# Performance work log

Hardware: AMD Instinct MI355X
Metric: run time of the kernel (lower is better)

## Reference

```python
import jax, jax.numpy as jnp
import numpy as np

MARGIN = 0.1
LAMDA = 1.0


def setup_inputs() -> dict:
    key = jax.random.key(0)
    k1, k2, k3 = jax.random.split(key, 3)
    B, C, D = 256, 4096, 100
    return {
        "feat_pos": jax.random.normal(k1, (B, D), dtype=jnp.float32),
        "feat_neg": jax.random.normal(k2, (B, C, D), dtype=jnp.float32),
        "feat_lan": jax.random.normal(k3, (B, D), dtype=jnp.float32),
    }


def reference(feat_pos, feat_neg, feat_lan):
    # loss1: overall mean squared distance between pos and lang features
    loss1 = jnp.mean((feat_pos - feat_lan) ** 2)
    # loss2: hinge on per-(b,c) mean squared distance pos vs each neg clip
    # d2[b, c] = mean_d (pos[b, d] - neg[b, c, d])^2
    d2 = jnp.mean((feat_pos[:, None, :] - feat_neg) ** 2, axis=-1)  # (B, C)
    loss2 = jnp.mean(jax.nn.relu(MARGIN - d2))  # sum / (B*C)
    return loss1 + LAMDA * loss2
```

## Files before the change

### kernel.cpp

```cpp
#include <hip/hip_runtime.h>

#define MARGIN 0.1f
#define BB 256
#define CC 4096
#define DD 100
#define TPB 256

__global__ __launch_bounds__(TPB) void amloss_kernel(const float* __restrict__ pos,
                                                     const float* __restrict__ neg,
                                                     const float* __restrict__ lan,
                                                     float* __restrict__ out) {
    const int tid = threadIdx.x;
    const int b   = blockIdx.y;
    const int c   = blockIdx.x * TPB + tid;

    __shared__ __align__(16) float pos_s[DD];
    if (tid < DD) pos_s[tid] = pos[b * DD + tid];
    __syncthreads();

    const float4* __restrict__ row =
        (const float4*)(neg + ((size_t)b * CC + (size_t)c) * DD);
    const float4* __restrict__ pos4 = (const float4*)pos_s;

    float s = 0.f;
    #pragma unroll
    for (int k = 0; k < DD / 4; ++k) {
        const float4 v = row[k];
        const float4 p = pos4[k];
        const float d0 = p.x - v.x;
        const float d1 = p.y - v.y;
        const float d2 = p.z - v.z;
        const float d3 = p.w - v.w;
        s += d0 * d0 + d1 * d1 + d2 * d2 + d3 * d3;
    }
    float contrib = fmaxf(MARGIN - s * (1.f / (float)DD), 0.f)
                  * (1.f / ((float)BB * (float)CC));

    if (blockIdx.x == 0 && tid < DD) {
        const float d = pos_s[tid] - lan[b * DD + tid];
        contrib += d * d * (1.f / ((float)BB * (float)DD));
    }

    #pragma unroll
    for (int off = 32; off >= 1; off >>= 1)
        contrib += __shfl_xor(contrib, off, 64);
    __shared__ float ws[4];
    if ((tid & 63) == 0) ws[tid >> 6] = contrib;
    __syncthreads();
    if (tid == 0) atomicAdd(out, ws[0] + ws[1] + ws[2] + ws[3]);
}

extern "C" void kernel_launch(void* const* d_in, const int* in_sizes, int n_in,
                              void* d_out, int out_size, void* d_ws, size_t ws_size,
                              hipStream_t stream) {
    const float* pos = (const float*)d_in[0];
    const float* neg = (const float*)d_in[1];
    const float* lan = (const float*)d_in[2];
    float* out = (float*)d_out;

    hipMemsetAsync(out, 0, (size_t)out_size * sizeof(float), stream);

    amloss_kernel<<<dim3(CC / TPB, BB), TPB, 0, stream>>>(pos, neg, lan, out);
}
```

Measured before the change: 573.6 us.

## Coalesce neg loads by striding threads across float4s with shared-memory row sums

Each thread used to read a whole 400-byte row on its own, so neighbouring lanes touched addresses 400 bytes apart and loads were poorly coalesced. Now the 256 threads walk the block's contiguous 256-row chunk float4 by float4, so lane reads are consecutive, and each partial sum is added into a per-row shared-memory accumulator with atomicAdd. This trades scattered global loads for many LDS atomics, with up to 25 lanes contending on the same row address, plus an extra barrier.

New measurement: 596.5 us. +4.0%, slower.

```diff
diff --git a/kernel.cpp b/kernel.cpp
--- a/kernel.cpp
+++ b/kernel.cpp
@@ -5,6 +5,9 @@
 #define CC 4096
 #define DD 100
 #define TPB 256
+#define ROWS 256
+#define F4_PER_ROW (DD / 4)
+#define ITERS (ROWS * F4_PER_ROW / TPB)
 
 __global__ __launch_bounds__(TPB) void amloss_kernel(const float* __restrict__ pos,
                                                      const float* __restrict__ neg,
@@ -12,28 +15,35 @@
                                                      float* __restrict__ out) {
     const int tid = threadIdx.x;
     const int b   = blockIdx.y;
-    const int c   = blockIdx.x * TPB + tid;
+    const int c0  = blockIdx.x * ROWS;
 
     __shared__ __align__(16) float pos_s[DD];
+    __shared__ float rowsum[ROWS];
+
+    rowsum[tid] = 0.f;
     if (tid < DD) pos_s[tid] = pos[b * DD + tid];
     __syncthreads();
 
-    const float4* __restrict__ row =
-        (const float4*)(neg + ((size_t)b * CC + (size_t)c) * DD);
+    const float4* __restrict__ nblk =
+        (const float4*)(neg + ((size_t)b * CC + (size_t)c0) * DD);
     const float4* __restrict__ pos4 = (const float4*)pos_s;
 
-    float s = 0.f;
-    #pragma unroll
-    for (int k = 0; k < DD / 4; ++k) {
-        const float4 v = row[k];
-        const float4 p = pos4[k];
+    #pragma unroll 5
+    for (int it = 0; it < ITERS; ++it) {
+        const int g   = it * TPB + tid;
+        const int row = g / F4_PER_ROW;
+        const int j   = g - row * F4_PER_ROW;
+        const float4 v = nblk[g];
+        const float4 p = pos4[j];
         const float d0 = p.x - v.x;
         const float d1 = p.y - v.y;
         const float d2 = p.z - v.z;
         const float d3 = p.w - v.w;
-        s += d0 * d0 + d1 * d1 + d2 * d2 + d3 * d3;
+        atomicAdd(&rowsum[row], d0 * d0 + d1 * d1 + d2 * d2 + d3 * d3);
     }
-    float contrib = fmaxf(MARGIN - s * (1.f / (float)DD), 0.f)
+    __syncthreads();
+
+    float contrib = fmaxf(MARGIN - rowsum[tid] * (1.f / (float)DD), 0.f)
                   * (1.f / ((float)BB * (float)CC));
 
     if (blockIdx.x == 0 && tid < DD) {
@@ -44,7 +54,7 @@
     #pragma unroll
     for (int off = 32; off >= 1; off >>= 1)
         contrib += __shfl_xor(contrib, off, 64);
-    __shared__ float ws[4];
+    __shared__ float ws[TPB / 64];
     if ((tid & 63) == 0) ws[tid >> 6] = contrib;
     __syncthreads();
     if (tid == 0) atomicAdd(out, ws[0] + ws[1] + ws[2] + ws[3]);
@@ -60,5 +70,5 @@
 
     hipMemsetAsync(out, 0, (size_t)out_size * sizeof(float), stream);
 
-    amloss_kernel<<<dim3(CC / TPB, BB), TPB, 0, stream>>>(pos, neg, lan, out);
+    amloss_kernel<<<dim3(CC / ROWS, BB), TPB, 0, stream>>>(pos, neg, lan, out);
 }
```
